# Performance work log

Hardware: AMD Instinct MI355X
Metric: run time of the kernel (lower is better)

The kernel has to match this reference:

```python
import jax, jax.numpy as jnp
import numpy as np

B, S, H, T = 32, 512, 256, 48
START_IDX, STOP_IDX = 46, 47
NEG = -10000.0


def setup_inputs() -> dict:
    key = jax.random.key(0)
    k1, k2, k3, k4, k5 = jax.random.split(key, 5)
    lstm_features = jax.random.normal(k1, (B, S, H), dtype=jnp.float32)
    emission_w = jax.random.normal(k2, (H, T), dtype=jnp.float32) * 0.02
    emission_b = jnp.zeros((T,), dtype=jnp.float32)
    transitions = jax.random.normal(k3, (T, T), dtype=jnp.float32)
    transitions = transitions.at[:, START_IDX].set(NEG).at[STOP_IDX, :].set(NEG)
    lengths = jax.random.randint(k4, (B,), S // 2, S + 1, dtype=jnp.int32)
    tags = jax.random.randint(k5, (B, S), 0, START_IDX, dtype=jnp.int32)
    return {
        'lstm_features': lstm_features,
        'emission_w': emission_w,
        'emission_b': emission_b,
        'transitions': transitions,
        'lengths': lengths,
        'tags': tags,
    }


def _crf_scores(lstm_features, emission_w, emission_b, transitions):
    # emission: [B,S,T] at the 'to' tag; crf[b,s,i,j] = emission[b,s,j] + transitions[i,j]
    em = jnp.einsum('bsh,ht->bst', lstm_features, emission_w) + emission_b
    return em[:, :, None, :] + transitions[None, None, :, :]


def _forward_alg(crf_scores, transitions, lengths):
    # alpha[b,j] = log-sum-exp over paths ending at tag j
    alpha0 = jnp.full((B, T), NEG, dtype=crf_scores.dtype).at[:, START_IDX].set(0.0)

    def step(alpha, xs):
        crf_t, t = xs  # crf_t: [B,T,T]
        tag_var = crf_t + alpha[:, :, None]  # add score of 'from' tag
        new_alpha = jax.scipy.special.logsumexp(tag_var, axis=1)  # reduce over 'from'
        alpha = jnp.where((t < lengths)[:, None], new_alpha, alpha)
        return alpha, None

    xs = (jnp.swapaxes(crf_scores, 0, 1), jnp.arange(S, dtype=lengths.dtype))
    alpha, _ = jax.lax.scan(step, alpha0, xs)
    terminal = alpha + transitions[:, STOP_IDX][None, :]
    return jax.scipy.special.logsumexp(terminal, axis=1)  # [B]


def _gold_score(crf_scores, transitions, tags, lengths):
    # from_tags[t] = START for t=0 else tags[t-1]; to_tags[t] = tags[t]
    start_col = jnp.full((B, 1), START_IDX, dtype=tags.dtype)
    from_tags = jnp.concatenate([start_col, tags[:, :-1]], axis=1)  # [B,S]
    b_idx = jnp.arange(B)[:, None]
    s_idx = jnp.arange(S)[None, :]
    sel = crf_scores[b_idx, s_idx, from_tags, tags]  # [B,S]
    mask = (s_idx < lengths[:, None]).astype(sel.dtype)
    last_tag = jnp.take_along_axis(tags, (lengths - 1)[:, None], axis=1)[:, 0]
    return jnp.sum(sel * mask, axis=1) + transitions[last_tag, STOP_IDX]  # [B]


def reference(lstm_features, emission_w, emission_b, transitions, lengths, tags):
    crf_scores = _crf_scores(lstm_features, emission_w, emission_b, transitions)
    all_paths = _forward_alg(crf_scores, transitions, lengths)
    gold = _gold_score(crf_scores, transitions, tags, lengths)
    return all_paths - gold  # per-example NLL, shape [B]
```

## Files before the change

### kernel.cpp

```cpp
#include <hip/hip_runtime.h>
#include <math.h>

#define BB 32
#define SS 512
#define HH 256
#define TT 48
#define START_IDX 46
#define STOP_IDX 47

typedef __attribute__((ext_vector_type(8))) short short8;
typedef __attribute__((ext_vector_type(4))) float floatx4;

__device__ __forceinline__ float rfl(float x) {
    return __int_as_float(__builtin_amdgcn_readfirstlane(__float_as_int(x)));
}
__device__ __forceinline__ unsigned int bf16_rne(float x) {
    const unsigned int u = __float_as_uint(x);
    return (u + 0x7fffu + ((u >> 16) & 1u)) >> 16;
}
__device__ __forceinline__ float bf2f(unsigned short h) {
    return __uint_as_float(((unsigned int)h) << 16);
}

__global__ __launch_bounds__(256) void prep_kernel(
    const float* __restrict__ w, const float* __restrict__ trans,
    uint4* __restrict__ Ebuf, uint4* __restrict__ Wbuf,
    float* __restrict__ goldb)
{
    __shared__ unsigned short wb[64 * 50];
    const int tid = threadIdx.x, blk = blockIdx.x;

    if (blk == 4) {
        if (tid < 32) goldb[tid] = 0.f;
        if (tid < 64) {
            const int g = tid >> 4, cl = tid & 15;
#pragma unroll
            for (int kc = 0; kc < 2; ++kc)
#pragma unroll
                for (int nt = 0; nt < 3; ++nt) {
                    unsigned int p[4];
#pragma unroll
                    for (int h2 = 0; h2 < 4; ++h2) {
                        const int k = kc * 32 + g * 8 + 2 * h2;
                        const int n = nt * 16 + cl;
                        const float lo = (k     < TT) ? __expf(trans[k * TT + n])       : 0.f;
                        const float hi = (k + 1 < TT) ? __expf(trans[(k + 1) * TT + n]) : 0.f;
                        p[h2] = bf16_rne(lo) | (bf16_rne(hi) << 16);
                    }
                    Ebuf[(kc * 3 + nt) * 64 + tid] = make_uint4(p[0], p[1], p[2], p[3]);
                }
        }
        return;
    }

    const int kt0 = blk * 2;
    const int R0  = kt0 * 32;
    for (int i = tid; i < 768; i += 256) {
        const float4 v = ((const float4*)w)[R0 * 12 + i];
        const int lr = i / 12, c4 = (i - lr * 12) * 4;
        unsigned short* d = &wb[lr * 50 + c4];
        d[0] = (unsigned short)bf16_rne(v.x);
        d[1] = (unsigned short)bf16_rne(v.y);
        d[2] = (unsigned short)bf16_rne(v.z);
        d[3] = (unsigned short)bf16_rne(v.w);
    }
    __syncthreads();
    for (int idx = tid; idx < 384; idx += 256) {
        const int fbl = idx >> 6, l = idx & 63;
        const int ktl = fbl / 3, nt = fbl - ktl * 3;
        const int kb  = ktl * 32 + (l >> 4) * 8;
        const int col = nt * 16 + (l & 15);
        unsigned int p[4];
#pragma unroll
        for (int h2 = 0; h2 < 4; ++h2) {
            const unsigned int lo = wb[(kb + 2 * h2)     * 50 + col];
            const unsigned int hi = wb[(kb + 2 * h2 + 1) * 50 + col];
            p[h2] = lo | (hi << 16);
        }
        Wbuf[((kt0 + ktl) * 3 + nt) * 64 + l] = make_uint4(p[0], p[1], p[2], p[3]);
    }
}

__global__ __launch_bounds__(192, 3) void fused_scan_kernel(
    const float* __restrict__ f, const float* __restrict__ bias,
    const float* __restrict__ trans, const int* __restrict__ lengths,
    const int* __restrict__ tags,
    unsigned short* __restrict__ Qs, float* __restrict__ Ls3,
    const uint4* __restrict__ Ebuf, const uint4* __restrict__ Wbuf,
    float* __restrict__ goldb, unsigned short* __restrict__ elast)
{
    __shared__ __align__(16) unsigned short ebuf[16 * TT];
    __shared__ __align__(16) unsigned short abuf[3][17 * 56];
    __shared__ __align__(16) float plds[16 * 48];

    const int bc = blockIdx.x, b = bc >> 5, c = bc & 31;
    const int len = lengths[b];
    const int tid = threadIdx.x, wv = tid >> 6, l = tid & 63, g = l >> 4, cl = l & 15;
    const int base16 = c << 4;

    const int nraw = (len - 1) - base16;
    if (nraw < 0) return;
    const int nsteps = (nraw > 16) ? 16 : nraw;

    {
        const float* frow = f + ((size_t)b * SS + base16 + cl) * HH + g * 8;
        float4 fv[8][2];
#pragma unroll
        for (int kt = 0; kt < 8; ++kt) {
            fv[kt][0] = *(const float4*)(frow + kt * 32);
            fv[kt][1] = *(const float4*)(frow + kt * 32 + 4);
        }
        uint4 wf[8];
#pragma unroll
        for (int kt = 0; kt < 8; ++kt) wf[kt] = Wbuf[(kt * 3 + wv) * 64 + l];

        floatx4 acc = {0.f, 0.f, 0.f, 0.f};
#pragma unroll
        for (int kt = 0; kt < 8; ++kt) {
            const unsigned int a0 = bf16_rne(fv[kt][0].x) | (bf16_rne(fv[kt][0].y) << 16);
            const unsigned int a1 = bf16_rne(fv[kt][0].z) | (bf16_rne(fv[kt][0].w) << 16);
            const unsigned int a2 = bf16_rne(fv[kt][1].x) | (bf16_rne(fv[kt][1].y) << 16);
            const unsigned int a3 = bf16_rne(fv[kt][1].z) | (bf16_rne(fv[kt][1].w) << 16);
            const short8 Af = __builtin_bit_cast(short8, make_uint4(a0, a1, a2, a3));
            acc = __builtin_amdgcn_mfma_f32_16x16x32_bf16(
                Af, __builtin_bit_cast(short8, wf[kt]), acc, 0, 0, 0);
        }
        const float bcol = bias[wv * 16 + cl];
#pragma unroll
        for (int r = 0; r < 4; ++r) {
            const int row = 4 * g + r, col = wv * 16 + cl;
            const float el = acc[r] + bcol;
            plds[row * 48 + col] = el;
            ebuf[row * TT + col] = (unsigned short)bf16_rne(__expf(el));
        }
    }
    __syncthreads();

    if (nraw <= 15 && tid < 24)
        ((unsigned int*)(elast + b * TT))[tid] = ((const unsigned int*)&ebuf[nraw * TT])[tid];

    if (wv == 0) {
        float gp = 0.f;
        if (l < 16) {
            const int s = base16 + l;
            if (s < len) {
                const int tag  = tags[b * SS + s];
                const int from = (s == 0) ? START_IDX : tags[b * SS + s - 1];
                gp = plds[l * 48 + tag] + trans[from * TT + tag];
            }
        }
        gp += __shfl_xor(gp, 8); gp += __shfl_xor(gp, 4);
        gp += __shfl_xor(gp, 2); gp += __shfl_xor(gp, 1);
        if (l == 0) atomicAdd(&goldb[b], gp);
    }

    if (nsteps > 0) {
        uint4 Bf[2][3];
#pragma unroll
        for (int kc = 0; kc < 2; ++kc)
#pragma unroll
            for (int nt = 0; nt < 3; ++nt)
                Bf[kc][nt] = Ebuf[(kc * 3 + nt) * 64 + l];

        floatx4 acc[3];
#pragma unroll
        for (int nt = 0; nt < 3; ++nt)
#pragma unroll
            for (int r = 0; r < 4; ++r)
                acc[nt][r] = (16 * wv + 4 * g + r == nt * 16 + cl) ? 1.f : 0.f;

        float ev[3];
#pragma unroll
        for (int nt = 0; nt < 3; ++nt) ev[nt] = bf2f(ebuf[nt * 16 + cl]);

        float Lrb = 0.f;
        unsigned short* aw = abuf[wv];

        for (int s = 0; s < nsteps; ++s) {
            float scale = 1.f;
            if (s == 8) {
                const float sig = rfl(acc[0][0]);
                Lrb = __logf(sig);
                scale = __builtin_amdgcn_rcpf(sig);
            }
            const float f0 = ev[0] * scale, f1 = ev[1] * scale, f2 = ev[2] * scale;
#pragma unroll
            for (int r = 0; r < 4; ++r) {
                const int rw = (4 * g + r) * 56;
                aw[rw +      cl] = (unsigned short)bf16_rne(acc[0][r] * f0);
                aw[rw + 16 + cl] = (unsigned short)bf16_rne(acc[1][r] * f1);
                aw[rw + 32 + cl] = (unsigned short)bf16_rne(acc[2][r] * f2);
            }
            if (s + 1 < nsteps) {
#pragma unroll
                for (int nt = 0; nt < 3; ++nt)
                    ev[nt] = bf2f(ebuf[(s + 1) * TT + nt * 16 + cl]);
            }
            uint4 a0 = *(const uint4*)&aw[cl * 56 + g * 8];
            uint4 a1 = *(const uint4*)&aw[cl * 56 + 32 + g * 8];
            if (g >= 2) a1 = make_uint4(0, 0, 0, 0);
            const floatx4 z = {0.f, 0.f, 0.f, 0.f};
#pragma unroll
            for (int nt = 0; nt < 3; ++nt) {
                floatx4 d = __builtin_amdgcn_mfma_f32_16x16x32_bf16(
                    __builtin_bit_cast(short8, a0), __builtin_bit_cast(short8, Bf[0][nt]), z, 0, 0, 0);
                d = __builtin_amdgcn_mfma_f32_16x16x32_bf16(
                    __builtin_bit_cast(short8, a1), __builtin_bit_cast(short8, Bf[1][nt]), d, 0, 0, 0);
                acc[nt] = d;
            }
        }

        unsigned short* qb = Qs + (size_t)bc * (TT * 64);
#pragma unroll
        for (int nt = 0; nt < 3; ++nt) {
            const unsigned int lo = bf16_rne(acc[nt][0]) | (bf16_rne(acc[nt][1]) << 16);
            const unsigned int hi = bf16_rne(acc[nt][2]) | (bf16_rne(acc[nt][3]) << 16);
            *(uint2*)&qb[(nt * 16 + cl) * 64 + 16 * wv + 4 * g] = make_uint2(lo, hi);
        }
        if (l == 0) Ls3[bc * 3 + wv] = Lrb;
    }
}

__global__ __launch_bounds__(256) void finalize_kernel(
    const float* __restrict__ trans,
    const int*   __restrict__ lengths,
    const int*   __restrict__ tags,
    const unsigned short* __restrict__ Qs,
    const float* __restrict__ Ls3,
    const float* __restrict__ goldb,
    const unsigned short* __restrict__ elast,
    float* __restrict__ out)
{
    __shared__ __align__(16) unsigned short Mlds[4][TT * 72];
    __shared__ __align__(16) unsigned short aw4[4][TT * 56 + 16];
    __shared__ float Lsl[96], fal[96], Lw[4];
    __shared__ __align__(16) unsigned short vlds[64];

    const int tid = threadIdx.x, b = blockIdx.x;
    const int wv = tid >> 6, l = tid & 63, g = l >> 4, cl = l & 15;

    const int len = lengths[b];
    const int nc = (len - 1 + 15) >> 4;

    if (tid < 96) Lsl[tid] = (tid < nc * 3) ? Ls3[b * 96 + tid] : 0.f;
    __syncthreads();
    if (tid < 96) fal[tid] = __expf(Lsl[tid] - Lsl[(tid / 3) * 3]);
    __syncthreads();

    const int K  = (nc + 3) >> 2;
    const int c0 = wv * K;
    const int c1 = (c0 + K < nc) ? (c0 + K) : nc;

    floatx4 M[3][3];
#pragma unroll
    for (int mt = 0; mt < 3; ++mt)
#pragma unroll
        for (int nt = 0; nt < 3; ++nt)
#pragma unroll
            for (int r = 0; r < 4; ++r)
                M[mt][nt][r] = (16 * mt + 4 * g + r == 16 * nt + cl) ? 1.f : 0.f;

    float inv = 1.f, Lacc = 0.f;
    unsigned short* aw = aw4[wv];
    const unsigned short* qbase = Qs + (size_t)(b * 32) * (TT * 64);

    uint4 pB0[3], pB1[3];
    if (c0 < c1) {
#pragma unroll
        for (int nt = 0; nt < 3; ++nt) {
            pB0[nt] = *(const uint4*)&qbase[(size_t)c0 * TT * 64 + (nt * 16 + cl) * 64 + g * 8];
            pB1[nt] = *(const uint4*)&qbase[(size_t)c0 * TT * 64 + (nt * 16 + cl) * 64 + 32 + g * 8];
        }
    }

    for (int c = c0; c < c1; ++c) {
        uint4 B0[3], B1[3];
#pragma unroll
        for (int nt = 0; nt < 3; ++nt) {
            B0[nt] = pB0[nt];
            B1[nt] = pB1[nt];
            if (g >= 2) B1[nt] = make_uint4(0, 0, 0, 0);
        }
        const int cn = (c + 1 < c1) ? c + 1 : c;
#pragma unroll
        for (int nt = 0; nt < 3; ++nt) {
            pB0[nt] = *(const uint4*)&qbase[(size_t)cn * TT * 64 + (nt * 16 + cl) * 64 + g * 8];
            pB1[nt] = *(const uint4*)&qbase[(size_t)cn * TT * 64 + (nt * 16 + cl) * 64 + 32 + g * 8];
        }

        const float f0 = inv * fal[c * 3 + 0];
        const float f1 = inv * fal[c * 3 + 1];
        const float f2 = inv * fal[c * 3 + 2];
        Lacc += Lsl[c * 3];

#pragma unroll
        for (int mt = 0; mt < 3; ++mt)
#pragma unroll
            for (int r = 0; r < 4; ++r) {
                const int rw = (16 * mt + 4 * g + r) * 56;
                aw[rw +      cl] = (unsigned short)bf16_rne(M[mt][0][r] * f0);
                aw[rw + 16 + cl] = (unsigned short)bf16_rne(M[mt][1][r] * f1);
                aw[rw + 32 + cl] = (unsigned short)bf16_rne(M[mt][2][r] * f2);
            }

        uint4 A0[3], A1[3];
#pragma unroll
        for (int mt = 0; mt < 3; ++mt) {
            A0[mt] = *(const uint4*)&aw[(16 * mt + cl) * 56 + g * 8];
            A1[mt] = *(const uint4*)&aw[(16 * mt + cl) * 56 + 32 + g * 8];
            if (g >= 2) A1[mt] = make_uint4(0, 0, 0, 0);
        }

        const floatx4 z = {0.f, 0.f, 0.f, 0.f};
#pragma unroll
        for (int mt = 0; mt < 3; ++mt)
#pragma unroll
            for (int nt = 0; nt < 3; ++nt) {
                floatx4 d = __builtin_amdgcn_mfma_f32_16x16x32_bf16(
                    __builtin_bit_cast(short8, A0[mt]), __builtin_bit_cast(short8, B0[nt]), z, 0, 0, 0);
                d = __builtin_amdgcn_mfma_f32_16x16x32_bf16(
                    __builtin_bit_cast(short8, A1[mt]), __builtin_bit_cast(short8, B1[nt]), d, 0, 0, 0);
                M[mt][nt] = d;
            }
        const float sig = rfl(M[0][0][0]);
        inv = __builtin_amdgcn_rcpf(sig);
        Lacc += __logf(sig);
    }

#pragma unroll
    for (int mt = 0; mt < 3; ++mt)
#pragma unroll
        for (int nt = 0; nt < 3; ++nt) {
            const unsigned int lo = bf16_rne(M[mt][nt][0] * inv) | (bf16_rne(M[mt][nt][1] * inv) << 16);
            const unsigned int hi = bf16_rne(M[mt][nt][2] * inv) | (bf16_rne(M[mt][nt][3] * inv) << 16);
            *(uint2*)&Mlds[wv][(nt * 16 + cl) * 72 + 16 * mt + 4 * g] = make_uint2(lo, hi);
        }
    if (l == 0) Lw[wv] = Lacc;
    __syncthreads();

    if (wv == 0) {
        const float vj = (l < TT) ? __expf(trans[START_IDX * TT + l]) : 0.f;
        vlds[l] = (unsigned short)bf16_rne(vj);

        float L = 0.f, cinv = 1.f;
        floatx4 accn[3];

        for (int w = 0; w < 4; ++w) {
            uint4 B0[3], B1[3];
#pragma unroll
            for (int nt = 0; nt < 3; ++nt) {
                B0[nt] = *(const uint4*)&Mlds[w][(nt * 16 + cl) * 72 + g * 8];
                B1[nt] = *(const uint4*)&Mlds[w][(nt * 16 + cl) * 72 + 32 + g * 8];
                if (g >= 2) B1[nt] = make_uint4(0, 0, 0, 0);
            }
            const uint4 A0 = *(const uint4*)&vlds[g * 8];
            const uint4 A1 = *(const uint4*)&vlds[32 + g * 8];

            const floatx4 z = {0.f, 0.f, 0.f, 0.f};
#pragma unroll
            for (int nt = 0; nt < 3; ++nt) {
                floatx4 d = __builtin_amdgcn_mfma_f32_16x16x32_bf16(
                    __builtin_bit_cast(short8, A0), __builtin_bit_cast(short8, B0[nt]), z, 0, 0, 0);
                d = __builtin_amdgcn_mfma_f32_16x16x32_bf16(
                    __builtin_bit_cast(short8, A1), __builtin_bit_cast(short8, B1[nt]), d, 0, 0, 0);
                accn[nt] = d;
            }
            const float sig = rfl(accn[0][0]);
            cinv = __builtin_amdgcn_rcpf(sig);
            L += __logf(sig) + Lw[w];
            if (w < 3 && l < 16) {
                vlds[ 0 + l] = (unsigned short)bf16_rne(accn[0][0] * cinv);
                vlds[16 + l] = (unsigned short)bf16_rne(accn[1][0] * cinv);
                vlds[32 + l] = (unsigned short)bf16_rne(accn[2][0] * cinv);
            }
        }

        float term = 0.f;
        if (l < 16) {
#pragma unroll
            for (int nt = 0; nt < 3; ++nt) {
                const int col = nt * 16 + l;
                term += accn[nt][0] * cinv * bf2f(elast[b * TT + col])
                        * __expf(trans[col * TT + STOP_IDX]);
            }
        }
        term += __shfl_xor(term, 32); term += __shfl_xor(term, 16); term += __shfl_xor(term, 8);
        term += __shfl_xor(term, 4);  term += __shfl_xor(term, 2);  term += __shfl_xor(term, 1);

        if (l == 0) {
            const float all_paths = __logf(term) + L;
            const int last = tags[b * SS + len - 1];
            out[b] = all_paths - (goldb[b] + trans[last * TT + STOP_IDX]);
        }
    }
}

extern "C" void kernel_launch(void* const* d_in, const int* in_sizes, int n_in,
                              void* d_out, int out_size, void* d_ws, size_t ws_size,
                              hipStream_t stream) {
    const float* f       = (const float*)d_in[0];
    const float* w       = (const float*)d_in[1];
    const float* bias    = (const float*)d_in[2];
    const float* trans   = (const float*)d_in[3];
    const int*   lengths = (const int*)d_in[4];
    const int*   tags    = (const int*)d_in[5];
    float*       out     = (float*)d_out;

    char* ws = (char*)d_ws;
    unsigned short* Qs   = (unsigned short*)ws;
    float*          Lsc  = (float*)(ws + 6291456);
    uint4*          Ebuf = (uint4*)(ws + 6303744);
    uint4*          Wbuf = (uint4*)(ws + 6309888);
    float*          goldb= (float*)(ws + 6334464);
    unsigned short* elast= (unsigned short*)(ws + 6334592);

    prep_kernel<<<5, 256, 0, stream>>>(w, trans, Ebuf, Wbuf, goldb);
    fused_scan_kernel<<<BB * 32, 192, 0, stream>>>(f, bias, trans, lengths, tags,
                                                   Qs, Lsc, Ebuf, Wbuf, goldb, elast);
    finalize_kernel<<<BB, 256, 0, stream>>>(trans, lengths, tags, Qs, Lsc, goldb, elast, out);
}
```

Baseline: 103.6 us.

## Fold prep kernel into scan kernel and drop gold-score atomics

Removes the separate prep launch. Each scan block now converts its slice of the emission weights and the exp(transitions) fragments to bf16 itself. Gold-score partials are written per block and reduced in finalize instead of using atomicAdd on a zeroed buffer. The first scan step is started directly from exp(transitions)·emission, and finalize starts its chunk product from the first Q chunk instead of an identity matrix, which skips one MFMA step in each. In exchange, every block redoes the weight and transition conversion with uncoalesced strided loads of w and trans.

```diff
diff --git a/kernel.cpp b/kernel.cpp
--- a/kernel.cpp
+++ b/kernel.cpp
@@ -22,76 +22,17 @@
     return __uint_as_float(((unsigned int)h) << 16);
 }
 
-__global__ __launch_bounds__(256) void prep_kernel(
-    const float* __restrict__ w, const float* __restrict__ trans,
-    uint4* __restrict__ Ebuf, uint4* __restrict__ Wbuf,
-    float* __restrict__ goldb)
-{
-    __shared__ unsigned short wb[64 * 50];
-    const int tid = threadIdx.x, blk = blockIdx.x;
-
-    if (blk == 4) {
-        if (tid < 32) goldb[tid] = 0.f;
-        if (tid < 64) {
-            const int g = tid >> 4, cl = tid & 15;
-#pragma unroll
-            for (int kc = 0; kc < 2; ++kc)
-#pragma unroll
-                for (int nt = 0; nt < 3; ++nt) {
-                    unsigned int p[4];
-#pragma unroll
-                    for (int h2 = 0; h2 < 4; ++h2) {
-                        const int k = kc * 32 + g * 8 + 2 * h2;
-                        const int n = nt * 16 + cl;
-                        const float lo = (k     < TT) ? __expf(trans[k * TT + n])       : 0.f;
-                        const float hi = (k + 1 < TT) ? __expf(trans[(k + 1) * TT + n]) : 0.f;
-                        p[h2] = bf16_rne(lo) | (bf16_rne(hi) << 16);
-                    }
-                    Ebuf[(kc * 3 + nt) * 64 + tid] = make_uint4(p[0], p[1], p[2], p[3]);
-                }
-        }
-        return;
-    }
-
-    const int kt0 = blk * 2;
-    const int R0  = kt0 * 32;
-    for (int i = tid; i < 768; i += 256) {
-        const float4 v = ((const float4*)w)[R0 * 12 + i];
-        const int lr = i / 12, c4 = (i - lr * 12) * 4;
-        unsigned short* d = &wb[lr * 50 + c4];
-        d[0] = (unsigned short)bf16_rne(v.x);
-        d[1] = (unsigned short)bf16_rne(v.y);
-        d[2] = (unsigned short)bf16_rne(v.z);
-        d[3] = (unsigned short)bf16_rne(v.w);
-    }
-    __syncthreads();
-    for (int idx = tid; idx < 384; idx += 256) {
-        const int fbl = idx >> 6, l = idx & 63;
-        const int ktl = fbl / 3, nt = fbl - ktl * 3;
-        const int kb  = ktl * 32 + (l >> 4) * 8;
-        const int col = nt * 16 + (l & 15);
-        unsigned int p[4];
-#pragma unroll
-        for (int h2 = 0; h2 < 4; ++h2) {
-            const unsigned int lo = wb[(kb + 2 * h2)     * 50 + col];
-            const unsigned int hi = wb[(kb + 2 * h2 + 1) * 50 + col];
-            p[h2] = lo | (hi << 16);
-        }
-        Wbuf[((kt0 + ktl) * 3 + nt) * 64 + l] = make_uint4(p[0], p[1], p[2], p[3]);
-    }
-}
-
 __global__ __launch_bounds__(192, 3) void fused_scan_kernel(
-    const float* __restrict__ f, const float* __restrict__ bias,
-    const float* __restrict__ trans, const int* __restrict__ lengths,
-    const int* __restrict__ tags,
+    const float* __restrict__ f, const float* __restrict__ w,
+    const float* __restrict__ bias, const float* __restrict__ trans,
+    const int* __restrict__ lengths, const int* __restrict__ tags,
     unsigned short* __restrict__ Qs, float* __restrict__ Ls3,
-    const uint4* __restrict__ Ebuf, const uint4* __restrict__ Wbuf,
-    float* __restrict__ goldb, unsigned short* __restrict__ elast)
+    float* __restrict__ goldp, unsigned short* __restrict__ elast)
 {
     __shared__ __align__(16) unsigned short ebuf[16 * TT];
     __shared__ __align__(16) unsigned short abuf[3][17 * 56];
     __shared__ __align__(16) float plds[16 * 48];
+    __shared__ __align__(16) uint4 efr[6 * 64];
 
     const int bc = blockIdx.x, b = bc >> 5, c = bc & 31;
     const int len = lengths[b];
@@ -99,28 +40,53 @@
     const int base16 = c << 4;
 
     const int nraw = (len - 1) - base16;
-    if (nraw < 0) return;
+    if (nraw < 0) {
+        if (tid == 0) goldp[bc] = 0.f;
+        return;
+    }
     const int nsteps = (nraw > 16) ? 16 : nraw;
 
+    if (nsteps > 1) {
+#pragma unroll
+        for (int kc = 0; kc < 2; ++kc) {
+            unsigned int p[4];
+#pragma unroll
+            for (int h2 = 0; h2 < 4; ++h2) {
+                const int k = kc * 32 + g * 8 + 2 * h2;
+                const int n = wv * 16 + cl;
+                const float lo = (k     < TT) ? __expf(trans[k * TT + n])       : 0.f;
+                const float hi = (k + 1 < TT) ? __expf(trans[(k + 1) * TT + n]) : 0.f;
+                p[h2] = bf16_rne(lo) | (bf16_rne(hi) << 16);
+            }
+            efr[(kc * 3 + wv) * 64 + l] = make_uint4(p[0], p[1], p[2], p[3]);
+        }
+    }
+
     {
+        const int wcol = wv * 16 + cl;
+        uint4 wf[8];
+#pragma unroll
+        for (int kt = 0; kt < 8; ++kt) {
+            unsigned int p[4];
+#pragma unroll
+            for (int h2 = 0; h2 < 4; ++h2) {
+                const int k = kt * 32 + g * 8 + 2 * h2;
+                p[h2] = bf16_rne(w[k * TT + wcol])
+                      | (bf16_rne(w[(k + 1) * TT + wcol]) << 16);
+            }
+            wf[kt] = make_uint4(p[0], p[1], p[2], p[3]);
+        }
+
         const float* frow = f + ((size_t)b * SS + base16 + cl) * HH + g * 8;
-        float4 fv[8][2];
+        floatx4 acc = {0.f, 0.f, 0.f, 0.f};
 #pragma unroll
         for (int kt = 0; kt < 8; ++kt) {
-            fv[kt][0] = *(const float4*)(frow + kt * 32);
-            fv[kt][1] = *(const float4*)(frow + kt * 32 + 4);
-        }
-        uint4 wf[8];
-#pragma unroll
-        for (int kt = 0; kt < 8; ++kt) wf[kt] = Wbuf[(kt * 3 + wv) * 64 + l];
-
-        floatx4 acc = {0.f, 0.f, 0.f, 0.f};
-#pragma unroll
-        for (int kt = 0; kt < 8; ++kt) {
-            const unsigned int a0 = bf16_rne(fv[kt][0].x) | (bf16_rne(fv[kt][0].y) << 16);
-            const unsigned int a1 = bf16_rne(fv[kt][0].z) | (bf16_rne(fv[kt][0].w) << 16);
-            const unsigned int a2 = bf16_rne(fv[kt][1].x) | (bf16_rne(fv[kt][1].y) << 16);
-            const unsigned int a3 = bf16_rne(fv[kt][1].z) | (bf16_rne(fv[kt][1].w) << 16);
+            const float4 v0 = *(const float4*)(frow + kt * 32);
+            const float4 v1 = *(const float4*)(frow + kt * 32 + 4);
+            const unsigned int a0 = bf16_rne(v0.x) | (bf16_rne(v0.y) << 16);
+            const unsigned int a1 = bf16_rne(v0.z) | (bf16_rne(v0.w) << 16);
+            const unsigned int a2 = bf16_rne(v1.x) | (bf16_rne(v1.y) << 16);
+            const unsigned int a3 = bf16_rne(v1.z) | (bf16_rne(v1.w) << 16);
             const short8 Af = __builtin_bit_cast(short8, make_uint4(a0, a1, a2, a3));
             acc = __builtin_amdgcn_mfma_f32_16x16x32_bf16(
                 Af, __builtin_bit_cast(short8, wf[kt]), acc, 0, 0, 0);
@@ -151,32 +117,36 @@
         }
         gp += __shfl_xor(gp, 8); gp += __shfl_xor(gp, 4);
         gp += __shfl_xor(gp, 2); gp += __shfl_xor(gp, 1);
-        if (l == 0) atomicAdd(&goldb[b], gp);
+        if (l == 0) goldp[bc] = gp;
     }
 
     if (nsteps > 0) {
+        floatx4 acc[3];
+#pragma unroll
+        for (int r = 0; r < 4; ++r) {
+            const int row = 16 * wv + 4 * g + r;
+            const float e0 = bf2f(ebuf[row]);
+#pragma unroll
+            for (int nt = 0; nt < 3; ++nt)
+                acc[nt][r] = e0 * __expf(trans[row * TT + nt * 16 + cl]);
+        }
+
+        float ev[3];
         uint4 Bf[2][3];
-#pragma unroll
-        for (int kc = 0; kc < 2; ++kc)
-#pragma unroll
-            for (int nt = 0; nt < 3; ++nt)
-                Bf[kc][nt] = Ebuf[(kc * 3 + nt) * 64 + l];
-
-        floatx4 acc[3];
-#pragma unroll
-        for (int nt = 0; nt < 3; ++nt)
-#pragma unroll
-            for (int r = 0; r < 4; ++r)
-                acc[nt][r] = (16 * wv + 4 * g + r == nt * 16 + cl) ? 1.f : 0.f;
-
-        float ev[3];
-#pragma unroll
-        for (int nt = 0; nt < 3; ++nt) ev[nt] = bf2f(ebuf[nt * 16 + cl]);
+        if (nsteps > 1) {
+#pragma unroll
+            for (int nt = 0; nt < 3; ++nt) ev[nt] = bf2f(ebuf[1 * TT + nt * 16 + cl]);
+#pragma unroll
+            for (int kc = 0; kc < 2; ++kc)
+#pragma unroll
+                for (int nt = 0; nt < 3; ++nt)
+                    Bf[kc][nt] = efr[(kc * 3 + nt) * 64 + l];
+        }
 
         float Lrb = 0.f;
         unsigned short* aw = abuf[wv];
 
-        for (int s = 0; s < nsteps; ++s) {
+        for (int s = 1; s < nsteps; ++s) {
             float scale = 1.f;
             if (s == 8) {
                 const float sig = rfl(acc[0][0]);
@@ -227,7 +197,7 @@
     const int*   __restrict__ tags,
     const unsigned short* __restrict__ Qs,
     const float* __restrict__ Ls3,
-    const float* __restrict__ goldb,
+    const float* __restrict__ goldp,
     const unsigned short* __restrict__ elast,
     float* __restrict__ out)
 {
@@ -235,6 +205,7 @@
     __shared__ __align__(16) unsigned short aw4[4][TT * 56 + 16];
     __shared__ float Lsl[96], fal[96], Lw[4];
     __shared__ __align__(16) unsigned short vlds[64];
+    __shared__ float goldtot;
 
     const int tid = threadIdx.x, b = blockIdx.x;
     const int wv = tid >> 6, l = tid & 63, g = l >> 4, cl = l & 15;
@@ -247,33 +218,52 @@
     if (tid < 96) fal[tid] = __expf(Lsl[tid] - Lsl[(tid / 3) * 3]);
     __syncthreads();
 
+    if (wv == 1) {
+        float gsum = (l < 32) ? goldp[b * 32 + l] : 0.f;
+        gsum += __shfl_xor(gsum, 16); gsum += __shfl_xor(gsum, 8);
+        gsum += __shfl_xor(gsum, 4);  gsum += __shfl_xor(gsum, 2);
+        gsum += __shfl_xor(gsum, 1);
+        if (l == 0) goldtot = gsum;
+    }
+
     const int K  = (nc + 3) >> 2;
     const int c0 = wv * K;
     const int c1 = (c0 + K < nc) ? (c0 + K) : nc;
+    const unsigned short* qbase = Qs + (size_t)(b * 32) * (TT * 64);
 
     floatx4 M[3][3];
-#pragma unroll
-    for (int mt = 0; mt < 3; ++mt)
-#pragma unroll
-        for (int nt = 0; nt < 3; ++nt)
-#pragma unroll
-            for (int r = 0; r < 4; ++r)
-                M[mt][nt][r] = (16 * mt + 4 * g + r == 16 * nt + cl) ? 1.f : 0.f;
-
-    float inv = 1.f, Lacc = 0.f;
+    {
+        const unsigned short* qb0 = qbase + (size_t)c0 * TT * 64;
+        const float fm0 = fal[c0 * 3 + 0], fm1 = fal[c0 * 3 + 1], fm2 = fal[c0 * 3 + 2];
+        const float fm[3] = {fm0, fm1, fm2};
+#pragma unroll
+        for (int mt = 0; mt < 3; ++mt)
+#pragma unroll
+            for (int nt = 0; nt < 3; ++nt) {
+                const uint2 q = *(const uint2*)&qb0[(nt * 16 + cl) * 64 + 16 * mt + 4 * g];
+                M[mt][nt][0] = bf2f((unsigned short)(q.x & 0xffffu)) * fm[mt];
+                M[mt][nt][1] = bf2f((unsigned short)(q.x >> 16))     * fm[mt];
+                M[mt][nt][2] = bf2f((unsigned short)(q.y & 0xffffu)) * fm[mt];
+                M[mt][nt][3] = bf2f((unsigned short)(q.y >> 16))     * fm[mt];
+            }
+    }
+    float Lacc = Lsl[c0 * 3];
+    const float sig0 = rfl(M[0][0][0]);
+    float inv = __builtin_amdgcn_rcpf(sig0);
+    Lacc += __logf(sig0);
+
     unsigned short* aw = aw4[wv];
-    const unsigned short* qbase = Qs + (size_t)(b * 32) * (TT * 64);
 
     uint4 pB0[3], pB1[3];
-    if (c0 < c1) {
+    if (c0 + 1 < c1) {
 #pragma unroll
         for (int nt = 0; nt < 3; ++nt) {
-            pB0[nt] = *(const uint4*)&qbase[(size_t)c0 * TT * 64 + (nt * 16 + cl) * 64 + g * 8];
-            pB1[nt] = *(const uint4*)&qbase[(size_t)c0 * TT * 64 + (nt * 16 + cl) * 64 + 32 + g * 8];
-        }
-    }
-
-    for (int c = c0; c < c1; ++c) {
+            pB0[nt] = *(const uint4*)&qbase[(size_t)(c0 + 1) * TT * 64 + (nt * 16 + cl) * 64 + g * 8];
+            pB1[nt] = *(const uint4*)&qbase[(size_t)(c0 + 1) * TT * 64 + (nt * 16 + cl) * 64 + 32 + g * 8];
+        }
+    }
+
+    for (int c = c0 + 1; c < c1; ++c) {
         uint4 B0[3], B1[3];
 #pragma unroll
         for (int nt = 0; nt < 3; ++nt) {
@@ -345,12 +335,12 @@
         float L = 0.f, cinv = 1.f;
         floatx4 accn[3];
 
-        for (int w = 0; w < 4; ++w) {
+        for (int w2 = 0; w2 < 4; ++w2) {
             uint4 B0[3], B1[3];
 #pragma unroll
             for (int nt = 0; nt < 3; ++nt) {
-                B0[nt] = *(const uint4*)&Mlds[w][(nt * 16 + cl) * 72 + g * 8];
-                B1[nt] = *(const uint4*)&Mlds[w][(nt * 16 + cl) * 72 + 32 + g * 8];
+                B0[nt] = *(const uint4*)&Mlds[w2][(nt * 16 + cl) * 72 + g * 8];
+                B1[nt] = *(const uint4*)&Mlds[w2][(nt * 16 + cl) * 72 + 32 + g * 8];
                 if (g >= 2) B1[nt] = make_uint4(0, 0, 0, 0);
             }
             const uint4 A0 = *(const uint4*)&vlds[g * 8];
@@ -367,8 +357,8 @@
             }
             const float sig = rfl(accn[0][0]);
             cinv = __builtin_amdgcn_rcpf(sig);
-            L += __logf(sig) + Lw[w];
-            if (w < 3 && l < 16) {
+            L += __logf(sig) + Lw[w2];
+            if (w2 < 3 && l < 16) {
                 vlds[ 0 + l] = (unsigned short)bf16_rne(accn[0][0] * cinv);
                 vlds[16 + l] = (unsigned short)bf16_rne(accn[1][0] * cinv);
                 vlds[32 + l] = (unsigned short)bf16_rne(accn[2][0] * cinv);
@@ -390,7 +380,7 @@
         if (l == 0) {
             const float all_paths = __logf(term) + L;
             const int last = tags[b * SS + len - 1];
-            out[b] = all_paths - (goldb[b] + trans[last * TT + STOP_IDX]);
+            out[b] = all_paths - (goldtot + trans[last * TT + STOP_IDX]);
         }
     }
 }
@@ -409,13 +399,10 @@
     char* ws = (char*)d_ws;
     unsigned short* Qs   = (unsigned short*)ws;
     float*          Lsc  = (float*)(ws + 6291456);
-    uint4*          Ebuf = (uint4*)(ws + 6303744);
-    uint4*          Wbuf = (uint4*)(ws + 6309888);
-    float*          goldb= (float*)(ws + 6334464);
-    unsigned short* elast= (unsigned short*)(ws + 6334592);
-
-    prep_kernel<<<5, 256, 0, stream>>>(w, trans, Ebuf, Wbuf, goldb);
-    fused_scan_kernel<<<BB * 32, 192, 0, stream>>>(f, bias, trans, lengths, tags,
-                                                   Qs, Lsc, Ebuf, Wbuf, goldb, elast);
-    finalize_kernel<<<BB, 256, 0, stream>>>(trans, lengths, tags, Qs, Lsc, goldb, elast, out);
-}
+    float*          goldp= (float*)(ws + 6303744);
+    unsigned short* elast= (unsigned short*)(ws + 6307840);
+
+    fused_scan_kernel<<<BB * 32, 192, 0, stream>>>(f, w, bias, trans, lengths, tags,
+                                                   Qs, Lsc, goldp, elast);
+    finalize_kernel<<<BB, 256, 0, stream>>>(trans, lengths, tags, Qs, Lsc, goldp, elast, out);
+}
```

Measured after the change: 99.37 us. 1.04x faster.
